# Kernel optimization log

Measured on AMD Instinct MI355X. Metric: run time of the kernel, lower is better.

## Reference

```python
import jax, jax.numpy as jnp
import numpy as np

NUM_EXPERTS = 3
INPUT_DIM = 1024
HIDDEN_DIM = 4096
OUTPUT_DIM = 1024
ROUTER_HIDDEN = 128
BATCH = 8192


def setup_inputs() -> dict:
    key = jax.random.key(0)
    ks = jax.random.split(key, 6)
    s_in = 1.0 / np.sqrt(INPUT_DIM)
    s_h = 1.0 / np.sqrt(HIDDEN_DIM)
    s_rh = 1.0 / np.sqrt(ROUTER_HIDDEN)
    return {
        "x": jax.random.normal(ks[0], (BATCH, INPUT_DIM), jnp.float32),
        "router_w1": jax.random.normal(ks[1], (INPUT_DIM, ROUTER_HIDDEN), jnp.float32) * s_in,
        "router_b1": jnp.zeros((ROUTER_HIDDEN,), jnp.float32),
        "router_w2": jax.random.normal(ks[2], (ROUTER_HIDDEN, NUM_EXPERTS), jnp.float32) * s_rh,
        "router_b2": jnp.zeros((NUM_EXPERTS,), jnp.float32),
        "expert_w1": jax.random.normal(ks[3], (NUM_EXPERTS, INPUT_DIM, HIDDEN_DIM), jnp.float32) * s_in,
        "expert_b1": jnp.zeros((NUM_EXPERTS, HIDDEN_DIM), jnp.float32),
        "expert_w2": jax.random.normal(ks[4], (NUM_EXPERTS, HIDDEN_DIM, OUTPUT_DIM), jnp.float32) * s_h,
        "expert_b2": jnp.zeros((NUM_EXPERTS, OUTPUT_DIM), jnp.float32),
    }


def reference(x, router_w1, router_b1, router_w2, router_b2,
              expert_w1, expert_b1, expert_w2, expert_b2):
    # Router: MLP -> softmax probs, hard top-1 selection (argmax)
    rh = jax.nn.relu(x @ router_w1 + router_b1)          # [B, 128]
    logits = rh @ router_w2 + router_b2                   # [B, E]
    probs = jax.nn.softmax(logits, axis=-1)
    selected = jnp.argmax(probs, axis=-1)                 # [B] int

    # Per-expert forward on all tokens (dense equivalent of masked dispatch)
    h = jax.nn.relu(jnp.einsum('bi,eih->ebh', x, expert_w1) + expert_b1[:, None, :])  # [E,B,H]
    y = jnp.einsum('ebh,eho->ebo', h, expert_w2) + expert_b2[:, None, :]              # [E,B,O]

    # Scatter-combine: each token takes its selected expert's output
    outputs = jnp.take_along_axis(
        y, selected[None, :, None], axis=0)[0]            # [B, O]

    # routing_stats: tokens per expert
    routing_stats = jnp.bincount(selected, length=NUM_EXPERTS)
    return outputs, routing_stats
```

## Files before the change

kernel.cpp:

```cpp
#include <hip/hip_runtime.h>
#include <hip/hip_bf16.h>

typedef short bf16x8 __attribute__((ext_vector_type(8)));
typedef float f32x4 __attribute__((ext_vector_type(4)));
typedef __attribute__((address_space(1))) const void gconst_t;
typedef __attribute__((address_space(3))) void lds_t;

#define DEVI __device__ __forceinline__

constexpr int BATCH   = 8192;
constexpr int IN_DIM  = 1024;
constexpr int HID     = 4096;
constexpr int OUT_DIM = 1024;
constexpr int NE      = 3;

constexpr size_t XBF_OFF  = 0;
constexpr size_t W1T_OFF  = 16777216;
constexpr size_t W2T_OFF  = W1T_OFF + 25165824;
constexpr size_t H_OFF    = W2T_OFF + 25165824;
constexpr size_t XLO_OFF  = H_OFF;
constexpr size_t META_OFF = H_OFF + 67108864;
constexpr size_t W3_OFF   = META_OFF + 131072;

DEVI unsigned short f2bf(float f) {
  __hip_bfloat16 h = __float2bfloat16(f);
  return *reinterpret_cast<unsigned short*>(&h);
}
DEVI float bf2f(unsigned short u) {
  unsigned v = (unsigned)u << 16;
  return __uint_as_float(v);
}

DEVI unsigned swz(unsigned b) { return b ^ (((b >> 7) & 7u) << 4); }

__global__ __launch_bounds__(256) void prepA_kernel(
    const float* __restrict__ x, const float* __restrict__ rw1,
    unsigned short* __restrict__ xb, unsigned short* __restrict__ xlo,
    unsigned short* __restrict__ w3) {
  __shared__ float tile[64][65];
  const int b = blockIdx.x;
  const int tid = threadIdx.x;
  if (b < 512) {
    const float4* xv4 = (const float4*)x;
    const int total = BATCH * IN_DIM / 4;
    for (int i = b * 256 + tid; i < total; i += 512 * 256) {
      const float4 v = xv4[i];
      ushort4 h, l;
      h.x = f2bf(v.x); l.x = f2bf(v.x - bf2f(h.x));
      h.y = f2bf(v.y); l.y = f2bf(v.y - bf2f(h.y));
      h.z = f2bf(v.z); l.z = f2bf(v.z - bf2f(h.z));
      h.w = f2bf(v.w); l.w = f2bf(v.w - bf2f(h.w));
      ((ushort4*)xb)[i] = h;
      ((ushort4*)xlo)[i] = l;
    }
  } else {
    const int w = b - 512;
    const int r0 = (w >> 1) * 64;
    const int c0 = (w & 1) * 64;
    const int tr = tid >> 4;
    const int tc = (tid & 15) << 2;
#pragma unroll
    for (int i = 0; i < 4; i++) {
      const int r = tr + i * 16;
      const float4 v = *(const float4*)(rw1 + (size_t)(r0 + r) * 128 + (c0 + tc));
      tile[r][tc + 0] = v.x; tile[r][tc + 1] = v.y; tile[r][tc + 2] = v.z; tile[r][tc + 3] = v.w;
    }
    __syncthreads();
#pragma unroll
    for (int i = 0; i < 4; i++) {
      const int c = tr + i * 16;
      ushort4 hi, lo;
      {
        float f;
        f = tile[tc + 0][c]; hi.x = f2bf(f); lo.x = f2bf(f - bf2f(hi.x));
        f = tile[tc + 1][c]; hi.y = f2bf(f); lo.y = f2bf(f - bf2f(hi.y));
        f = tile[tc + 2][c]; hi.z = f2bf(f); lo.z = f2bf(f - bf2f(hi.z));
        f = tile[tc + 3][c]; hi.w = f2bf(f); lo.w = f2bf(f - bf2f(hi.w));
      }
      unsigned short* base = w3 + (size_t)(c0 + c) * 3072 + (r0 + tc);
      *(ushort4*)(base)        = hi;
      *(ushort4*)(base + 1024) = hi;
      *(ushort4*)(base + 2048) = lo;
    }
  }
}

__global__ __launch_bounds__(256) void router_gemm(
    const unsigned short* __restrict__ xhi, const unsigned short* __restrict__ xlo,
    const unsigned short* __restrict__ w3, const float* __restrict__ rb1,
    const float* __restrict__ rw2, const float* __restrict__ rb2,
    int* __restrict__ counts, int* __restrict__ toklist) {
  __shared__ __align__(16) char smem[70656];
  unsigned short* Ab = (unsigned short*)smem;
  unsigned short* Bb = (unsigned short*)(smem + 24576);
  float* rhp  = (float*)smem;
  float* lgp  = (float*)(smem + 67584);
  float* rw2l = (float*)(smem + 69120);

  const int tid = threadIdx.x;
  const int m0 = blockIdx.x * 128;
  constexpr int NT = 96;

  int tokA[2], kelA[2];
  unsigned aoff[2];
  const unsigned short* bsrc[2];
  unsigned boff[2];
#pragma unroll
  for (int l = 0; l < 2; l++) {
    const unsigned o = l * 4096u + (unsigned)tid * 16u;
    const unsigned p = swz(o);
    const int row = (int)(p >> 6);
    const int kel = (int)((p & 63u) >> 1);
    aoff[l] = o;
    tokA[l] = m0 + row;
    kelA[l] = kel;
    boff[l] = o;
    bsrc[l] = w3 + (size_t)row * 3072 + kel;
  }

  auto STAGE = [&](int buf, int t) {
    const int seg = t >> 5;
    const int kin = (t & 31) * 32;
    const unsigned short* abase = (seg == 1) ? xlo : xhi;
#pragma unroll
    for (int l = 0; l < 2; l++)
      __builtin_amdgcn_global_load_lds(
          (gconst_t*)(abase + (size_t)tokA[l] * 1024 + kin + kelA[l]),
          (lds_t*)((char*)Ab + buf * 8192 + aoff[l]), 16, 0, 0);
#pragma unroll
    for (int l = 0; l < 2; l++)
      __builtin_amdgcn_global_load_lds(
          (gconst_t*)(bsrc[l] + t * 32),
          (lds_t*)((char*)Bb + buf * 8192 + boff[l]), 16, 0, 0);
  };

  f32x4 acc[4][4];
#pragma unroll
  for (int i = 0; i < 4; i++)
#pragma unroll
    for (int j = 0; j < 4; j++) acc[i][j] = {0.f, 0.f, 0.f, 0.f};

  const int lane = tid & 63;
  const int wave = tid >> 6;
  const int wm = (wave >> 1) * 64;
  const int wn = (wave & 1) * 64;
  const int fr = lane & 15;
  const int fc = lane >> 4;

  STAGE(0, 0);
  STAGE(1, 1);

  int cur = 0;
  for (int t = 0; t < NT; ++t) {
    if (t + 1 < NT) asm volatile("s_waitcnt vmcnt(4)" ::: "memory");
    else            asm volatile("s_waitcnt vmcnt(0)" ::: "memory");
    __builtin_amdgcn_sched_barrier(0);
    __builtin_amdgcn_s_barrier();
    __builtin_amdgcn_sched_barrier(0);
    if (t + 2 < NT) {
      const int nb = (cur + 2 >= 3) ? cur - 1 : cur + 2;
      STAGE(nb, t + 2);
    }
    bf16x8 af[4], bv[4];
#pragma unroll
    for (int m = 0; m < 4; m++) {
      const unsigned L = (unsigned)(wm + m * 16 + fr) * 64u + (unsigned)(fc << 4);
      af[m] = *(const bf16x8*)((const char*)Ab + cur * 8192 + swz(L));
    }
#pragma unroll
    for (int n = 0; n < 4; n++) {
      const unsigned L = (unsigned)(wn + n * 16 + fr) * 64u + (unsigned)(fc << 4);
      bv[n] = *(const bf16x8*)((const char*)Bb + cur * 8192 + swz(L));
    }
    __builtin_amdgcn_s_setprio(1);
#pragma unroll
    for (int m = 0; m < 4; m++)
#pragma unroll
      for (int n = 0; n < 4; n++)
        acc[m][n] = __builtin_amdgcn_mfma_f32_16x16x32_bf16(af[m], bv[n], acc[m][n], 0, 0, 0);
    __builtin_amdgcn_s_setprio(0);
    cur = (cur + 1 == 3) ? 0 : cur + 1;
  }

  __syncthreads();

  for (int i = tid; i < 384; i += 256) rw2l[i] = rw2[i];

  const int crow = (lane >> 4) * 4;
  const int ccol = lane & 15;
  float b1v[4];
#pragma unroll
  for (int ni = 0; ni < 4; ni++) b1v[ni] = rb1[wn + ni * 16 + ccol];
#pragma unroll
  for (int mi = 0; mi < 4; mi++) {
#pragma unroll
    for (int r = 0; r < 4; r++) {
      const int tokL = wm + mi * 16 + crow + r;
#pragma unroll
      for (int ni = 0; ni < 4; ni++) {
        const int h = wn + ni * 16 + ccol;
        rhp[tokL * 132 + h] = fmaxf(acc[mi][ni][r] + b1v[ni], 0.f);
      }
    }
  }
  __syncthreads();

#pragma unroll
  for (int pass = 0; pass < 2; ++pass) {
    const int t = tid + pass * 256;
    if (t < 384) {
      const int tok = t / 3, e = t - tok * 3;
      float s = rb2[e];
#pragma unroll 4
      for (int j = 0; j < 128; ++j) s = fmaf(rhp[tok * 132 + j], rw2l[j * 3 + e], s);
      lgp[tok * 3 + e] = s;
    }
  }
  __syncthreads();

  if (tid < 128) {
    const float l0 = lgp[tid * 3], l1 = lgp[tid * 3 + 1], l2 = lgp[tid * 3 + 2];
    int sel = 0; float m = l0;
    if (l1 > m) { m = l1; sel = 1; }
    if (l2 > m) { m = l2; sel = 2; }
    const int slot = atomicAdd(&counts[sel], 1);
    toklist[sel * BATCH + slot] = m0 + tid;
  }
}

__global__ __launch_bounds__(256) void prep2_kernel(
    const float* __restrict__ ew1, const float* __restrict__ ew2,
    unsigned short* __restrict__ w1t, unsigned short* __restrict__ w2t) {
  __shared__ float tile[64][65];
  const int b = blockIdx.x;
  const int tid = threadIdx.x;

  const float* src; unsigned short* dst; int R, C, r0, c0;
  if (b < 3072) {
    const int e = b / 1024, w = b % 1024;
    src = ew1 + (size_t)e * 1024 * 4096; dst = w1t + (size_t)e * 4096 * 1024;
    R = 1024; C = 4096; r0 = (w & 15) * 64; c0 = (w >> 4) * 64;
  } else {
    const int bb = b - 3072, e = bb / 1024, w = bb % 1024;
    src = ew2 + (size_t)e * 4096 * 1024; dst = w2t + (size_t)e * 1024 * 4096;
    R = 4096; C = 1024; r0 = (w & 63) * 64; c0 = (w >> 6) * 64;
  }
  const int tr = tid >> 4;
  const int tc = (tid & 15) << 2;
#pragma unroll
  for (int i = 0; i < 4; i++) {
    const int r = tr + i * 16;
    const float4 v = *(const float4*)(src + (size_t)(r0 + r) * C + (c0 + tc));
    tile[r][tc + 0] = v.x; tile[r][tc + 1] = v.y; tile[r][tc + 2] = v.z; tile[r][tc + 3] = v.w;
  }
  __syncthreads();
#pragma unroll
  for (int i = 0; i < 4; i++) {
    const int c = tr + i * 16;
    ushort4 o;
    o.x = f2bf(tile[tc + 0][c]);
    o.y = f2bf(tile[tc + 1][c]);
    o.z = f2bf(tile[tc + 2][c]);
    o.w = f2bf(tile[tc + 3][c]);
    *(ushort4*)(dst + (size_t)(c0 + c) * R + (r0 + tc)) = o;
  }
}

template <int MODE>
__global__ __launch_bounds__(512, 2) void moe_gemm(
    const unsigned short* __restrict__ Abase, const unsigned short* __restrict__ Ball,
    const float* __restrict__ biasAll, unsigned short* __restrict__ Hout,
    float* __restrict__ Yout, const int* __restrict__ toklist, const int* __restrict__ counts,
    float* __restrict__ tail) {
  constexpr int N  = (MODE == 0) ? HID : OUT_DIM;
  constexpr int K  = (MODE == 0) ? IN_DIM : HID;
  constexpr int NT = K / 32;

  const int tid = threadIdx.x;
  if (MODE == 0 && blockIdx.x == 0 && blockIdx.y == 0 && tid < NE)
    tail[tid] = (float)counts[tid];

  const int c0 = counts[0], c1 = counts[1], c2 = counts[2];
  const int mb0 = (c0 + 127) >> 7, mb1 = (c1 + 127) >> 7, mb2 = (c2 + 127) >> 7;
  const int bx = blockIdx.x;
  int e, mblk;
  if (bx < mb0) { e = 0; mblk = bx; }
  else if (bx < mb0 + mb1) { e = 1; mblk = bx - mb0; }
  else if (bx < mb0 + mb1 + mb2) { e = 2; mblk = bx - mb0 - mb1; }
  else return;
  const int cnt = (e == 0) ? c0 : (e == 1) ? c1 : c2;
  const int m0 = mblk * 128;
  const int n0 = blockIdx.y * 256;
  const int off_e = (e > 0 ? c0 : 0) + (e > 1 ? c1 : 0);
  const unsigned short* Bmat = Ball + (size_t)e * ((size_t)N * K);
  const float* bias = biasAll + (size_t)e * N;

  __shared__ unsigned short Ab[3][128 * 32];
  __shared__ unsigned short Bb[3][256 * 32];

  const unsigned short* asrc;
  const unsigned short* bsrc[2];
  unsigned aoff, boff[2];
  {
    const unsigned o = (unsigned)tid * 16u;
    const unsigned p = swz(o);
    const int row = (int)(p >> 6);
    const int kel = (int)((p & 63u) >> 1);
    aoff = o;
    int slot = m0 + row; if (slot > cnt - 1) slot = cnt - 1;
    const size_t arow = (MODE == 0) ? (size_t)toklist[e * BATCH + slot]
                                    : (size_t)(off_e + slot);
    asrc = Abase + arow * K + kel;
  }
#pragma unroll
  for (int l = 0; l < 2; l++) {
    const unsigned o = l * 8192u + (unsigned)tid * 16u;
    const unsigned p = swz(o);
    const int row = (int)(p >> 6);
    const int kel = (int)((p & 63u) >> 1);
    boff[l] = o;
    bsrc[l] = Bmat + (size_t)(n0 + row) * K + kel;
  }

  f32x4 acc[4][4];
#pragma unroll
  for (int i = 0; i < 4; i++)
#pragma unroll
    for (int j = 0; j < 4; j++) acc[i][j] = {0.f, 0.f, 0.f, 0.f};

  const int lane = tid & 63;
  const int wave = tid >> 6;
  const int wm = (wave >> 2) * 64;
  const int wn = (wave & 3) * 64;
  const int fr = lane & 15;
  const int fc = lane >> 4;

  auto STAGE = [&](int buf, int kofs) {
    __builtin_amdgcn_global_load_lds((gconst_t*)(asrc + kofs),
                                     (lds_t*)((char*)&Ab[buf][0] + aoff), 16, 0, 0);
#pragma unroll
    for (int l = 0; l < 2; l++)
      __builtin_amdgcn_global_load_lds((gconst_t*)(bsrc[l] + kofs),
                                       (lds_t*)((char*)&Bb[buf][0] + boff[l]), 16, 0, 0);
  };

  STAGE(0, 0);
  STAGE(1, 32);

  int cur = 0;
  for (int t = 0; t < NT; ++t) {
    if (t + 1 < NT) asm volatile("s_waitcnt vmcnt(3)" ::: "memory");
    else            asm volatile("s_waitcnt vmcnt(0)" ::: "memory");
    __builtin_amdgcn_sched_barrier(0);
    __builtin_amdgcn_s_barrier();
    __builtin_amdgcn_sched_barrier(0);
    if (t + 2 < NT) {
      const int nb = (cur + 2 >= 3) ? cur - 1 : cur + 2;
      STAGE(nb, (t + 2) * 32);
    }
    bf16x8 af[4], bv[4];
#pragma unroll
    for (int m = 0; m < 4; m++) {
      const unsigned L = (unsigned)(wm + m * 16 + fr) * 64u + (unsigned)(fc << 4);
      af[m] = *(const bf16x8*)((const char*)&Ab[cur][0] + swz(L));
    }
#pragma unroll
    for (int n = 0; n < 4; n++) {
      const unsigned L = (unsigned)(wn + n * 16 + fr) * 64u + (unsigned)(fc << 4);
      bv[n] = *(const bf16x8*)((const char*)&Bb[cur][0] + swz(L));
    }
    __builtin_amdgcn_s_setprio(1);
#pragma unroll
    for (int m = 0; m < 4; m++)
#pragma unroll
      for (int n = 0; n < 4; n++)
        acc[m][n] = __builtin_amdgcn_mfma_f32_16x16x32_bf16(af[m], bv[n], acc[m][n], 0, 0, 0);
    __builtin_amdgcn_s_setprio(0);
    cur = (cur + 1 == 3) ? 0 : cur + 1;
  }

  const int crow = (lane >> 4) * 4;
  const int ccol = lane & 15;
#pragma unroll
  for (int mi = 0; mi < 4; mi++) {
#pragma unroll
    for (int r = 0; r < 4; r++) {
      const int slot = m0 + wm + mi * 16 + crow + r;
      if (slot >= cnt) continue;
      if (MODE == 0) {
        unsigned short* hrow = Hout + (size_t)(off_e + slot) * HID;
#pragma unroll
        for (int ni = 0; ni < 4; ni++) {
          const int n = n0 + wn + ni * 16 + ccol;
          const float v = acc[mi][ni][r] + bias[n];
          hrow[n] = f2bf(fmaxf(v, 0.f));
        }
      } else {
        const int tok = toklist[e * BATCH + slot];
        float* yrow = Yout + (size_t)tok * OUT_DIM;
#pragma unroll
        for (int ni = 0; ni < 4; ni++) {
          const int n = n0 + wn + ni * 16 + ccol;
          yrow[n] = acc[mi][ni][r] + bias[n];
        }
      }
    }
  }
}

extern "C" void kernel_launch(void* const* d_in, const int* in_sizes, int n_in,
                              void* d_out, int out_size, void* d_ws, size_t ws_size,
                              hipStream_t stream) {
  const float* x   = (const float*)d_in[0];
  const float* rw1 = (const float*)d_in[1];
  const float* rb1 = (const float*)d_in[2];
  const float* rw2 = (const float*)d_in[3];
  const float* rb2 = (const float*)d_in[4];
  const float* ew1 = (const float*)d_in[5];
  const float* eb1 = (const float*)d_in[6];
  const float* ew2 = (const float*)d_in[7];
  const float* eb2 = (const float*)d_in[8];
  float* out = (float*)d_out;

  char* ws = (char*)d_ws;
  unsigned short* xb  = (unsigned short*)(ws + XBF_OFF);
  unsigned short* w1t = (unsigned short*)(ws + W1T_OFF);
  unsigned short* w2t = (unsigned short*)(ws + W2T_OFF);
  unsigned short* h   = (unsigned short*)(ws + H_OFF);
  unsigned short* xlo = (unsigned short*)(ws + XLO_OFF);
  int* counts  = (int*)(ws + META_OFF);
  int* toklist = counts + 16;
  unsigned short* w3 = (unsigned short*)(ws + W3_OFF);
  float* tail = out + (size_t)BATCH * OUT_DIM;

  hipMemsetAsync(counts, 0, 64, stream);
  prepA_kernel<<<544, 256, 0, stream>>>(x, rw1, xb, xlo, w3);
  router_gemm<<<64, 256, 0, stream>>>(xb, xlo, w3, rb1, rw2, rb2, counts, toklist);
  prep2_kernel<<<6144, 256, 0, stream>>>(ew1, ew2, w1t, w2t);
  moe_gemm<0><<<dim3(66, 16), 512, 0, stream>>>(xb, w1t, eb1, h, nullptr, toklist, counts, tail);
  moe_gemm<1><<<dim3(66, 4), 512, 0, stream>>>(h, w2t, eb2, nullptr, out, toklist, counts, tail);
}
```

Before: 376.2 us.

## Split router GEMM across K segments and simplify MoE GEMM to single-buffered 128x128 tiles

The router GEMM is split into a 3-way K-split kernel that writes fp32 partial sums to workspace, followed by a finish kernel that reduces the partials, applies bias, ReLU and the second layer, and routes tokens. This raises router parallelism from 64 blocks to 192. The MoE GEMMs drop the 3-stage async pipeline with 128x256 tiles and 512 threads for a single-buffered 128x128 tile with K=64 steps and 256 threads, which doubles the grid. In exchange, global loads no longer overlap with MFMA work, and the router adds an extra kernel launch plus a round trip of the partials through workspace.

```diff
diff --git a/kernel.cpp b/kernel.cpp
--- a/kernel.cpp
+++ b/kernel.cpp
@@ -19,6 +19,7 @@
 constexpr size_t W2T_OFF  = W1T_OFF + 25165824;
 constexpr size_t H_OFF    = W2T_OFF + 25165824;
 constexpr size_t XLO_OFF  = H_OFF;
+constexpr size_t RHP_OFF  = H_OFF + 16777216;
 constexpr size_t META_OFF = H_OFF + 67108864;
 constexpr size_t W3_OFF   = META_OFF + 131072;
 
@@ -85,54 +86,30 @@
   }
 }
 
-__global__ __launch_bounds__(256) void router_gemm(
+__global__ __launch_bounds__(256) void router_part(
     const unsigned short* __restrict__ xhi, const unsigned short* __restrict__ xlo,
-    const unsigned short* __restrict__ w3, const float* __restrict__ rb1,
-    const float* __restrict__ rw2, const float* __restrict__ rb2,
-    int* __restrict__ counts, int* __restrict__ toklist) {
-  __shared__ __align__(16) char smem[70656];
-  unsigned short* Ab = (unsigned short*)smem;
-  unsigned short* Bb = (unsigned short*)(smem + 24576);
-  float* rhp  = (float*)smem;
-  float* lgp  = (float*)(smem + 67584);
-  float* rw2l = (float*)(smem + 69120);
-
+    const unsigned short* __restrict__ w3, float* __restrict__ rhpart) {
+  __shared__ unsigned short At[128 * 64];
+  __shared__ unsigned short Bt[128 * 64];
   const int tid = threadIdx.x;
   const int m0 = blockIdx.x * 128;
-  constexpr int NT = 96;
-
-  int tokA[2], kelA[2];
-  unsigned aoff[2];
-  const unsigned short* bsrc[2];
-  unsigned boff[2];
-#pragma unroll
-  for (int l = 0; l < 2; l++) {
+  const int seg = blockIdx.y;
+  const unsigned short* Abase = (seg == 1) ? xlo : xhi;
+  const int kcol0 = seg * 1024;
+
+  const unsigned short* asrc[4];
+  const unsigned short* bsrc[4];
+  unsigned loff[4];
+#pragma unroll
+  for (int l = 0; l < 4; l++) {
     const unsigned o = l * 4096u + (unsigned)tid * 16u;
     const unsigned p = swz(o);
-    const int row = (int)(p >> 6);
-    const int kel = (int)((p & 63u) >> 1);
-    aoff[l] = o;
-    tokA[l] = m0 + row;
-    kelA[l] = kel;
-    boff[l] = o;
-    bsrc[l] = w3 + (size_t)row * 3072 + kel;
-  }
-
-  auto STAGE = [&](int buf, int t) {
-    const int seg = t >> 5;
-    const int kin = (t & 31) * 32;
-    const unsigned short* abase = (seg == 1) ? xlo : xhi;
-#pragma unroll
-    for (int l = 0; l < 2; l++)
-      __builtin_amdgcn_global_load_lds(
-          (gconst_t*)(abase + (size_t)tokA[l] * 1024 + kin + kelA[l]),
-          (lds_t*)((char*)Ab + buf * 8192 + aoff[l]), 16, 0, 0);
-#pragma unroll
-    for (int l = 0; l < 2; l++)
-      __builtin_amdgcn_global_load_lds(
-          (gconst_t*)(bsrc[l] + t * 32),
-          (lds_t*)((char*)Bb + buf * 8192 + boff[l]), 16, 0, 0);
-  };
+    const int row = (int)(o >> 7);
+    const int kel = (int)((p & 127u) >> 1);
+    loff[l] = o;
+    asrc[l] = Abase + (size_t)(m0 + row) * 1024 + kel;
+    bsrc[l] = w3 + (size_t)row * 3072 + kcol0 + kel;
+  }
 
   f32x4 acc[4][4];
 #pragma unroll
@@ -147,64 +124,78 @@
   const int fr = lane & 15;
   const int fc = lane >> 4;
 
-  STAGE(0, 0);
-  STAGE(1, 1);
-
-  int cur = 0;
-  for (int t = 0; t < NT; ++t) {
-    if (t + 1 < NT) asm volatile("s_waitcnt vmcnt(4)" ::: "memory");
-    else            asm volatile("s_waitcnt vmcnt(0)" ::: "memory");
-    __builtin_amdgcn_sched_barrier(0);
-    __builtin_amdgcn_s_barrier();
-    __builtin_amdgcn_sched_barrier(0);
-    if (t + 2 < NT) {
-      const int nb = (cur + 2 >= 3) ? cur - 1 : cur + 2;
-      STAGE(nb, t + 2);
-    }
-    bf16x8 af[4], bv[4];
-#pragma unroll
-    for (int m = 0; m < 4; m++) {
-      const unsigned L = (unsigned)(wm + m * 16 + fr) * 64u + (unsigned)(fc << 4);
-      af[m] = *(const bf16x8*)((const char*)Ab + cur * 8192 + swz(L));
-    }
-#pragma unroll
-    for (int n = 0; n < 4; n++) {
-      const unsigned L = (unsigned)(wn + n * 16 + fr) * 64u + (unsigned)(fc << 4);
-      bv[n] = *(const bf16x8*)((const char*)Bb + cur * 8192 + swz(L));
-    }
-    __builtin_amdgcn_s_setprio(1);
-#pragma unroll
-    for (int m = 0; m < 4; m++)
-#pragma unroll
-      for (int n = 0; n < 4; n++)
-        acc[m][n] = __builtin_amdgcn_mfma_f32_16x16x32_bf16(af[m], bv[n], acc[m][n], 0, 0, 0);
-    __builtin_amdgcn_s_setprio(0);
-    cur = (cur + 1 == 3) ? 0 : cur + 1;
-  }
-
-  __syncthreads();
-
-  for (int i = tid; i < 384; i += 256) rw2l[i] = rw2[i];
+  for (int t = 0; t < 16; ++t) {
+    __syncthreads();
+#pragma unroll
+    for (int l = 0; l < 4; l++) {
+      __builtin_amdgcn_global_load_lds((gconst_t*)(asrc[l] + t * 64),
+                                       (lds_t*)((char*)At + loff[l]), 16, 0, 0);
+      __builtin_amdgcn_global_load_lds((gconst_t*)(bsrc[l] + t * 64),
+                                       (lds_t*)((char*)Bt + loff[l]), 16, 0, 0);
+    }
+    __syncthreads();
+    bf16x8 af[2][4], bv[2][4];
+#pragma unroll
+    for (int ks = 0; ks < 2; ks++) {
+#pragma unroll
+      for (int m = 0; m < 4; m++) {
+        const unsigned L = (unsigned)(wm + m * 16 + fr) * 128u + (unsigned)(ks * 64 + fc * 16);
+        af[ks][m] = *(const bf16x8*)((const char*)At + swz(L));
+      }
+#pragma unroll
+      for (int n = 0; n < 4; n++) {
+        const unsigned L = (unsigned)(wn + n * 16 + fr) * 128u + (unsigned)(ks * 64 + fc * 16);
+        bv[ks][n] = *(const bf16x8*)((const char*)Bt + swz(L));
+      }
+    }
+#pragma unroll
+    for (int ks = 0; ks < 2; ks++)
+#pragma unroll
+      for (int m = 0; m < 4; m++)
+#pragma unroll
+        for (int n = 0; n < 4; n++)
+          acc[m][n] = __builtin_amdgcn_mfma_f32_16x16x32_bf16(af[ks][m], bv[ks][n], acc[m][n], 0, 0, 0);
+  }
 
   const int crow = (lane >> 4) * 4;
   const int ccol = lane & 15;
-  float b1v[4];
-#pragma unroll
-  for (int ni = 0; ni < 4; ni++) b1v[ni] = rb1[wn + ni * 16 + ccol];
+  float* outp = rhpart + (size_t)seg * BATCH * 128;
 #pragma unroll
   for (int mi = 0; mi < 4; mi++) {
 #pragma unroll
     for (int r = 0; r < 4; r++) {
-      const int tokL = wm + mi * 16 + crow + r;
-#pragma unroll
-      for (int ni = 0; ni < 4; ni++) {
-        const int h = wn + ni * 16 + ccol;
-        rhp[tokL * 132 + h] = fmaxf(acc[mi][ni][r] + b1v[ni], 0.f);
-      }
-    }
+      const int tok = m0 + wm + mi * 16 + crow + r;
+#pragma unroll
+      for (int ni = 0; ni < 4; ni++)
+        outp[(size_t)tok * 128 + (wn + ni * 16 + ccol)] = acc[mi][ni][r];
+    }
+  }
+}
+
+__global__ __launch_bounds__(256) void router_finish(
+    const float* __restrict__ rhpart, const float* __restrict__ rb1,
+    const float* __restrict__ rw2, const float* __restrict__ rb2,
+    int* __restrict__ counts, int* __restrict__ toklist) {
+  __shared__ float rh[128 * 132];
+  __shared__ float lg[128 * 3];
+  const int tid = threadIdx.x;
+  const int t0 = blockIdx.x * 128;
+  constexpr size_t SEG = (size_t)BATCH * 128;
+
+  for (int i = tid; i < 128 * 32; i += 256) {
+    const int tok = i >> 5;
+    const int c4 = (i & 31) * 4;
+    const size_t base = (size_t)(t0 + tok) * 128 + c4;
+    const float4 a = *(const float4*)(rhpart + base);
+    const float4 b = *(const float4*)(rhpart + SEG + base);
+    const float4 c = *(const float4*)(rhpart + 2 * SEG + base);
+    const float4 bb = *(const float4*)(rb1 + c4);
+    rh[tok * 132 + c4 + 0] = fmaxf(a.x + b.x + c.x + bb.x, 0.f);
+    rh[tok * 132 + c4 + 1] = fmaxf(a.y + b.y + c.y + bb.y, 0.f);
+    rh[tok * 132 + c4 + 2] = fmaxf(a.z + b.z + c.z + bb.z, 0.f);
+    rh[tok * 132 + c4 + 3] = fmaxf(a.w + b.w + c.w + bb.w, 0.f);
   }
   __syncthreads();
-
 #pragma unroll
   for (int pass = 0; pass < 2; ++pass) {
     const int t = tid + pass * 256;
@@ -212,19 +203,18 @@
       const int tok = t / 3, e = t - tok * 3;
       float s = rb2[e];
 #pragma unroll 4
-      for (int j = 0; j < 128; ++j) s = fmaf(rhp[tok * 132 + j], rw2l[j * 3 + e], s);
-      lgp[tok * 3 + e] = s;
+      for (int j = 0; j < 128; ++j) s = fmaf(rh[tok * 132 + j], rw2[j * 3 + e], s);
+      lg[tok * 3 + e] = s;
     }
   }
   __syncthreads();
-
   if (tid < 128) {
-    const float l0 = lgp[tid * 3], l1 = lgp[tid * 3 + 1], l2 = lgp[tid * 3 + 2];
+    const float l0 = lg[tid * 3], l1 = lg[tid * 3 + 1], l2 = lg[tid * 3 + 2];
     int sel = 0; float m = l0;
     if (l1 > m) { m = l1; sel = 1; }
     if (l2 > m) { m = l2; sel = 2; }
     const int slot = atomicAdd(&counts[sel], 1);
-    toklist[sel * BATCH + slot] = m0 + tid;
+    toklist[sel * BATCH + slot] = t0 + tid;
   }
 }
 
@@ -267,14 +257,14 @@
 }
 
 template <int MODE>
-__global__ __launch_bounds__(512, 2) void moe_gemm(
+__global__ __launch_bounds__(256) void moe_gemm(
     const unsigned short* __restrict__ Abase, const unsigned short* __restrict__ Ball,
     const float* __restrict__ biasAll, unsigned short* __restrict__ Hout,
     float* __restrict__ Yout, const int* __restrict__ toklist, const int* __restrict__ counts,
     float* __restrict__ tail) {
   constexpr int N  = (MODE == 0) ? HID : OUT_DIM;
   constexpr int K  = (MODE == 0) ? IN_DIM : HID;
-  constexpr int NT = K / 32;
+  constexpr int NT = K / 64;
 
   const int tid = threadIdx.x;
   if (MODE == 0 && blockIdx.x == 0 && blockIdx.y == 0 && tid < NE)
@@ -290,35 +280,28 @@
   else return;
   const int cnt = (e == 0) ? c0 : (e == 1) ? c1 : c2;
   const int m0 = mblk * 128;
-  const int n0 = blockIdx.y * 256;
+  const int n0 = blockIdx.y * 128;
   const int off_e = (e > 0 ? c0 : 0) + (e > 1 ? c1 : 0);
   const unsigned short* Bmat = Ball + (size_t)e * ((size_t)N * K);
   const float* bias = biasAll + (size_t)e * N;
 
-  __shared__ unsigned short Ab[3][128 * 32];
-  __shared__ unsigned short Bb[3][256 * 32];
-
-  const unsigned short* asrc;
-  const unsigned short* bsrc[2];
-  unsigned aoff, boff[2];
-  {
-    const unsigned o = (unsigned)tid * 16u;
+  __shared__ unsigned short At[128 * 64];
+  __shared__ unsigned short Bt[128 * 64];
+
+  const unsigned short* asrc[4];
+  const unsigned short* bsrc[4];
+  unsigned loff[4];
+#pragma unroll
+  for (int l = 0; l < 4; l++) {
+    const unsigned o = l * 4096u + (unsigned)tid * 16u;
     const unsigned p = swz(o);
-    const int row = (int)(p >> 6);
-    const int kel = (int)((p & 63u) >> 1);
-    aoff = o;
+    const int row = (int)(o >> 7);
+    const int kel = (int)((p & 127u) >> 1);
+    loff[l] = o;
     int slot = m0 + row; if (slot > cnt - 1) slot = cnt - 1;
     const size_t arow = (MODE == 0) ? (size_t)toklist[e * BATCH + slot]
                                     : (size_t)(off_e + slot);
-    asrc = Abase + arow * K + kel;
-  }
-#pragma unroll
-  for (int l = 0; l < 2; l++) {
-    const unsigned o = l * 8192u + (unsigned)tid * 16u;
-    const unsigned p = swz(o);
-    const int row = (int)(p >> 6);
-    const int kel = (int)((p & 63u) >> 1);
-    boff[l] = o;
+    asrc[l] = Abase + arow * K + kel;
     bsrc[l] = Bmat + (size_t)(n0 + row) * K + kel;
   }
 
@@ -330,53 +313,42 @@
 
   const int lane = tid & 63;
   const int wave = tid >> 6;
-  const int wm = (wave >> 2) * 64;
-  const int wn = (wave & 3) * 64;
+  const int wm = (wave >> 1) * 64;
+  const int wn = (wave & 1) * 64;
   const int fr = lane & 15;
   const int fc = lane >> 4;
 
-  auto STAGE = [&](int buf, int kofs) {
-    __builtin_amdgcn_global_load_lds((gconst_t*)(asrc + kofs),
-                                     (lds_t*)((char*)&Ab[buf][0] + aoff), 16, 0, 0);
-#pragma unroll
-    for (int l = 0; l < 2; l++)
-      __builtin_amdgcn_global_load_lds((gconst_t*)(bsrc[l] + kofs),
-                                       (lds_t*)((char*)&Bb[buf][0] + boff[l]), 16, 0, 0);
-  };
-
-  STAGE(0, 0);
-  STAGE(1, 32);
-
-  int cur = 0;
   for (int t = 0; t < NT; ++t) {
-    if (t + 1 < NT) asm volatile("s_waitcnt vmcnt(3)" ::: "memory");
-    else            asm volatile("s_waitcnt vmcnt(0)" ::: "memory");
-    __builtin_amdgcn_sched_barrier(0);
-    __builtin_amdgcn_s_barrier();
-    __builtin_amdgcn_sched_barrier(0);
-    if (t + 2 < NT) {
-      const int nb = (cur + 2 >= 3) ? cur - 1 : cur + 2;
-      STAGE(nb, (t + 2) * 32);
-    }
-    bf16x8 af[4], bv[4];
-#pragma unroll
-    for (int m = 0; m < 4; m++) {
-      const unsigned L = (unsigned)(wm + m * 16 + fr) * 64u + (unsigned)(fc << 4);
-      af[m] = *(const bf16x8*)((const char*)&Ab[cur][0] + swz(L));
-    }
-#pragma unroll
-    for (int n = 0; n < 4; n++) {
-      const unsigned L = (unsigned)(wn + n * 16 + fr) * 64u + (unsigned)(fc << 4);
-      bv[n] = *(const bf16x8*)((const char*)&Bb[cur][0] + swz(L));
-    }
-    __builtin_amdgcn_s_setprio(1);
-#pragma unroll
-    for (int m = 0; m < 4; m++)
-#pragma unroll
-      for (int n = 0; n < 4; n++)
-        acc[m][n] = __builtin_amdgcn_mfma_f32_16x16x32_bf16(af[m], bv[n], acc[m][n], 0, 0, 0);
-    __builtin_amdgcn_s_setprio(0);
-    cur = (cur + 1 == 3) ? 0 : cur + 1;
+    __syncthreads();
+#pragma unroll
+    for (int l = 0; l < 4; l++) {
+      __builtin_amdgcn_global_load_lds((gconst_t*)(asrc[l] + t * 64),
+                                       (lds_t*)((char*)At + loff[l]), 16, 0, 0);
+      __builtin_amdgcn_global_load_lds((gconst_t*)(bsrc[l] + t * 64),
+                                       (lds_t*)((char*)Bt + loff[l]), 16, 0, 0);
+    }
+    __syncthreads();
+    bf16x8 af[2][4], bv[2][4];
+#pragma unroll
+    for (int ks = 0; ks < 2; ks++) {
+#pragma unroll
+      for (int m = 0; m < 4; m++) {
+        const unsigned L = (unsigned)(wm + m * 16 + fr) * 128u + (unsigned)(ks * 64 + fc * 16);
+        af[ks][m] = *(const bf16x8*)((const char*)At + swz(L));
+      }
+#pragma unroll
+      for (int n = 0; n < 4; n++) {
+        const unsigned L = (unsigned)(wn + n * 16 + fr) * 128u + (unsigned)(ks * 64 + fc * 16);
+        bv[ks][n] = *(const bf16x8*)((const char*)Bt + swz(L));
+      }
+    }
+#pragma unroll
+    for (int ks = 0; ks < 2; ks++)
+#pragma unroll
+      for (int m = 0; m < 4; m++)
+#pragma unroll
+        for (int n = 0; n < 4; n++)
+          acc[m][n] = __builtin_amdgcn_mfma_f32_16x16x32_bf16(af[ks][m], bv[ks][n], acc[m][n], 0, 0, 0);
   }
 
   const int crow = (lane >> 4) * 4;
@@ -428,6 +400,7 @@
   unsigned short* w2t = (unsigned short*)(ws + W2T_OFF);
   unsigned short* h   = (unsigned short*)(ws + H_OFF);
   unsigned short* xlo = (unsigned short*)(ws + XLO_OFF);
+  float* rhpart = (float*)(ws + RHP_OFF);
   int* counts  = (int*)(ws + META_OFF);
   int* toklist = counts + 16;
   unsigned short* w3 = (unsigned short*)(ws + W3_OFF);
@@ -435,8 +408,9 @@
 
   hipMemsetAsync(counts, 0, 64, stream);
   prepA_kernel<<<544, 256, 0, stream>>>(x, rw1, xb, xlo, w3);
-  router_gemm<<<64, 256, 0, stream>>>(xb, xlo, w3, rb1, rw2, rb2, counts, toklist);
+  router_part<<<dim3(64, 3), 256, 0, stream>>>(xb, xlo, w3, rhpart);
+  router_finish<<<64, 256, 0, stream>>>(rhpart, rb1, rw2, rb2, counts, toklist);
   prep2_kernel<<<6144, 256, 0, stream>>>(ew1, ew2, w1t, w2t);
-  moe_gemm<0><<<dim3(66, 16), 512, 0, stream>>>(xb, w1t, eb1, h, nullptr, toklist, counts, tail);
-  moe_gemm<1><<<dim3(66, 4), 512, 0, stream>>>(h, w2t, eb2, nullptr, out, toklist, counts, tail);
-}
+  moe_gemm<0><<<dim3(66, 32), 256, 0, stream>>>(xb, w1t, eb1, h, nullptr, toklist, counts, tail);
+  moe_gemm<1><<<dim3(66, 8), 256, 0, stream>>>(h, w2t, eb2, nullptr, out, toklist, counts, tail);
+}
```

Measured after the change: 411.1 us. 1.09x slower.
